# Optimization experiments

Hardware: AMD Instinct MI355X
Metric: run time of the kernel (lower is better)

The kernel has to match this reference:

```python
import jax, jax.numpy as jnp
import numpy as np
from jax import lax

KS, STRIDE, DIL, PAD = 3, 1, 1, 1
B, C_IN, C_OUT, D = 1, 16, 16, 64
K = KS ** 3


def setup_inputs():
    key = jax.random.key(0)
    k1, k2, k3 = jax.random.split(key, 3)
    x = jax.random.normal(k1, (B, C_IN, D, D, D), jnp.float32)
    std = 1.0 / float(np.sqrt(C_IN * K))
    kernel = jax.random.uniform(k2, (K, C_IN, C_OUT), jnp.float32, -std, std)
    # module zero-inits pkernel; use small random values so interp path is exercised
    pkernel = jax.random.normal(k3, (K, C_IN, 3 * K), jnp.float32) * 0.01
    return {"x": x, "kernel": kernel, "pkernel": pkernel}


def _deform_conv3d(x, kernel, pkernel):
    Bn, C, Dd, H, W = x.shape
    Kt = kernel.shape[0]
    # offset-predicting conv: pkernel [K, C_in, 3K] -> conv weight [3K, C_in, kd, kh, kw]
    w_off = jnp.transpose(pkernel.reshape(KS, KS, KS, C, 3 * Kt), (4, 3, 0, 1, 2))
    off = lax.conv_general_dilated(
        x, w_off, (STRIDE,) * 3, [(PAD, PAD)] * 3,
        rhs_dilation=(DIL,) * 3,
        dimension_numbers=("NCDHW", "OIDHW", "NCDHW"))
    Do, Ho, Wo = off.shape[2], off.shape[3], off.shape[4]
    off = off.reshape(Bn, Kt, 3, Do, Ho, Wo)  # 3 offset coords per kernel tap

    # base sampling grid: out_pos*stride - pad + tap*dilation, then add predicted offset
    r = jnp.arange(KS)
    tap = jnp.stack(jnp.meshgrid(r, r, r, indexing="ij"), -1).reshape(Kt, 3) * DIL - PAD
    gz = (jnp.arange(Do) * STRIDE).astype(x.dtype)
    gy = (jnp.arange(Ho) * STRIDE).astype(x.dtype)
    gx = (jnp.arange(Wo) * STRIDE).astype(x.dtype)
    cz = gz[None, None, :, None, None] + tap[None, :, 0, None, None, None] + off[:, :, 0]
    cy = gy[None, None, None, :, None] + tap[None, :, 1, None, None, None] + off[:, :, 1]
    cx = gx[None, None, None, None, :] + tap[None, :, 2, None, None, None] + off[:, :, 2]

    x_flat = x.reshape(Bn, C, Dd * H * W)

    def gather(idx):  # idx [B,K,Do,Ho,Wo] int32 -> [B,C,K,Do,Ho,Wo]
        g = jax.vmap(lambda xf, ix: xf[:, ix.reshape(-1)])(x_flat, idx)
        return g.reshape(Bn, C, Kt, Do, Ho, Wo)

    z0f = jnp.floor(cz); y0f = jnp.floor(cy); x0f = jnp.floor(cx)
    fz, fy, fx = cz - z0f, cy - y0f, cx - x0f
    z0 = z0f.astype(jnp.int32); y0 = y0f.astype(jnp.int32); x0 = x0f.astype(jnp.int32)

    # trilinear interp: accumulate 8 corners (zero outside volume)
    acc = jnp.zeros((Bn, C, Kt, Do, Ho, Wo), x.dtype)
    for dz in (0, 1):
        for dy in (0, 1):
            for dx in (0, 1):
                zi, yi, xi = z0 + dz, y0 + dy, x0 + dx
                valid = ((zi >= 0) & (zi < Dd) & (yi >= 0) & (yi < H)
                         & (xi >= 0) & (xi < W)).astype(x.dtype)
                w = ((fz if dz else 1.0 - fz) * (fy if dy else 1.0 - fy)
                     * (fx if dx else 1.0 - fx)) * valid
                idx = (jnp.clip(zi, 0, Dd - 1) * (H * W)
                       + jnp.clip(yi, 0, H - 1) * W + jnp.clip(xi, 0, W - 1))
                acc = acc + gather(idx) * w[:, None]

    # weighted sum over taps: kernel [K, C_in, C_out]
    return jnp.einsum("bckdhw,kco->bodhw", acc, kernel)


def reference(x, kernel, pkernel):
    return _deform_conv3d(x, kernel, pkernel)
```

## Files before the change

kernel.cpp:

```cpp
#include <hip/hip_runtime.h>

#define D 64
#define DD 4096
#define DDD 262144
#define K 27

typedef _Float16 half8  __attribute__((ext_vector_type(8)));
typedef _Float16 half2v __attribute__((ext_vector_type(2)));
typedef float    f32x4  __attribute__((ext_vector_type(4)));
typedef float    f32x2  __attribute__((ext_vector_type(2)));
typedef float    f32x16 __attribute__((ext_vector_type(16)));

#define HX 12
#define HY 8
#define HZ 6
#define HROW 12
#define HPLN 96
#define HSP  576
#define CPAD 24
#define VSLOT 24

#define WSW_CH (14*6*64)
#define KSW_CH (27*64)
#define KSW_OFF 88064

__device__ inline half2v h2of(half8 v, int d) {
    half2v r; r.x = v[2*d]; r.y = v[2*d+1]; return r;
}

__global__ __launch_bounds__(256) void prep_weights(const float* __restrict__ pk,
                                                    const float* __restrict__ kern,
                                                    _Float16* __restrict__ Wsw,
                                                    _Float16* __restrict__ Ksw) {
    int t = blockIdx.x * 256 + threadIdx.x;
    if (t < WSW_CH) {
        int lane = t & 63;
        int sm = t >> 6;
        int s = sm / 6, mt = sm - 6 * s;
        int m = mt * 16 + (lane & 15);
        int q = lane >> 4;
        half8 w;
#pragma unroll
        for (int j = 0; j < 8; ++j) {
            int k = 32 * s + 8 * q + j;
            int kt = k >> 4, c = k & 15;
            float wv = (kt < K && m < 81) ? pk[kt * 1296 + c * 81 + m] : 0.0f;
            w[j] = (_Float16)wv;
        }
        *(half8*)(Wsw + t * 8) = w;
    } else if (t < WSW_CH + KSW_CH) {
        int u = t - WSW_CH;
        int kt = u >> 6, lane = u & 63;
        int m = lane & 31, kh = lane >> 5;
        half8 w;
#pragma unroll
        for (int j = 0; j < 8; ++j) {
            int c = kh * 8 + j;
            float wv = (m < 16) ? kern[kt * 256 + c * 16 + m] : 0.0f;
            w[j] = (_Float16)wv;
        }
        *(half8*)(Ksw + u * 8) = w;
    }
}

__global__ __launch_bounds__(256, 3) void deform_main(
    const float* __restrict__ x,
    const _Float16* __restrict__ Wsw,
    const _Float16* __restrict__ Ksw,
    float* __restrict__ out)
{
    __shared__ _Float16 s_h[HSP * CPAD];
    __shared__ _Float16 s_off[81 * 64];
    __shared__ _Float16 s_v[4 * 64 * VSLOT];

    const int tid  = threadIdx.x;
    const int lane = tid & 63;
    const int wave = __builtin_amdgcn_readfirstlane(tid >> 6);

    const int bx0 = blockIdx.x * 8;
    const int by0 = blockIdx.y * 4;
    const int bz0 = blockIdx.z * 2;

    for (int i = tid; i < HSP; i += 256) {
        int z = i / HPLN;
        int r = i - z * HPLN;
        int y = r / HROW;
        int xx = r - y * HROW;
        int gz = bz0 - 2 + z, gy = by0 - 2 + y, gx = bx0 - 2 + xx;
        bool in = (unsigned)gz < D && (unsigned)gy < D && (unsigned)gx < D;
        half8 a = {}, b = {};
        if (in) {
            const float* p = x + (gz * DD + gy * D + gx);
#pragma unroll
            for (int c = 0; c < 8; ++c) a[c] = (_Float16)p[c * DDD];
#pragma unroll
            for (int c = 0; c < 8; ++c) b[c] = (_Float16)p[(c + 8) * DDD];
        }
        *(half8*)(s_h + i * CPAD)     = a;
        *(half8*)(s_h + i * CPAD + 8) = b;
    }
    __syncthreads();

    {
        const int n = lane & 15, q = lane >> 4;
        const int vtz = wave >> 1;
        const int vty = 2 * (wave & 1) + (n >> 3);
        const int vtx = n & 7;
        f32x4 acc[6] = {};
        for (int s = 0; s < 14; ++s) {
            int kt = 2 * s + (q >> 1);
            int ktc = (kt < K) ? kt : 0;
            int kd = ktc / 9, kh = (ktc / 3) % 3, kw = ktc % 3;
            int idx = (vtz + kd + 1) * HPLN + (vty + kh + 1) * HROW + (vtx + kw + 1);
            half8 bfrag = *(const half8*)(s_h + idx * CPAD + (q & 1) * 8);
#pragma unroll
            for (int mt = 0; mt < 6; ++mt) {
                half8 afrag = *(const half8*)(Wsw + ((s * 6 + mt) * 64 + lane) * 8);
                acc[mt] = __builtin_amdgcn_mfma_f32_16x16x32_f16(afrag, bfrag, acc[mt], 0, 0, 0);
            }
        }
        const int v = wave * 16 + n;
#pragma unroll
        for (int mt = 0; mt < 6; ++mt)
#pragma unroll
            for (int r = 0; r < 4; ++r) {
                int o = mt * 16 + q * 4 + r;
                if (o < 81) s_off[o * 64 + v] = (_Float16)acc[mt][r];
            }
    }
    __syncthreads();

    const int tx = lane & 7, ty = (lane >> 3) & 3, tz = lane >> 5;
    const int gz = bz0 + tz, gy = by0 + ty, gx = bx0 + tx;
    const int l31 = lane & 31, lh = lane >> 5;
    _Float16* sv = s_v + wave * 64 * VSLOT;

    f32x16 acc2[2] = {};

    const int ntaps = (wave < 3) ? 7 : 6;
    for (int t = 0; t < ntaps; ++t) {
        const int kt = wave * 7 + t;
        const int kd = kt / 9, kh = (kt / 3) % 3, kw = kt % 3;
        float cz = (float)(gz + kd - 1) + (float)s_off[(3 * kt + 0) * 64 + lane];
        float cy = (float)(gy + kh - 1) + (float)s_off[(3 * kt + 1) * 64 + lane];
        float cx = (float)(gx + kw - 1) + (float)s_off[(3 * kt + 2) * 64 + lane];
        float zf = floorf(cz), yf = floorf(cy), xf = floorf(cx);
        float fz = cz - zf, fy = cy - yf, fx = cx - xf;
        int z0 = (int)zf, y0 = (int)yf, x0 = (int)xf;
        int hz0 = z0 - bz0 + 2, hy0 = y0 - by0 + 2, hx0 = x0 - bx0 + 2;

        half2v val2[8] = {};
        if ((unsigned)hz0 < (unsigned)(HZ - 1) && (unsigned)hy0 < (unsigned)(HY - 1)
            && (unsigned)hx0 < (unsigned)(HX - 1)) {
#pragma unroll
            for (int dz = 0; dz < 2; ++dz) {
                float wz = dz ? fz : 1.0f - fz;
#pragma unroll
                for (int dy = 0; dy < 2; ++dy) {
                    float wzy = wz * (dy ? fy : 1.0f - fy);
#pragma unroll
                    for (int dx = 0; dx < 2; ++dx) {
                        float w = wzy * (dx ? fx : 1.0f - fx);
                        int idx = (hz0 + dz) * HPLN + (hy0 + dy) * HROW + (hx0 + dx);
                        half8 c0 = *(const half8*)(s_h + idx * CPAD);
                        half8 c1 = *(const half8*)(s_h + idx * CPAD + 8);
                        _Float16 wh = (_Float16)w;
                        half2v w2; w2.x = wh; w2.y = wh;
#pragma unroll
                        for (int d = 0; d < 4; ++d)
                            val2[d] += w2 * h2of(c0, d);
#pragma unroll
                        for (int d = 0; d < 4; ++d)
                            val2[d + 4] += w2 * h2of(c1, d);
                    }
                }
            }
        } else {
            f32x2 valf[8] = {};
#pragma unroll
            for (int dz = 0; dz < 2; ++dz) {
                int zi = z0 + dz;
                float wz = dz ? fz : 1.0f - fz;
#pragma unroll
                for (int dy = 0; dy < 2; ++dy) {
                    int yi = y0 + dy;
                    float wzy = wz * (dy ? fy : 1.0f - fy);
#pragma unroll
                    for (int dx = 0; dx < 2; ++dx) {
                        int xi = x0 + dx;
                        if ((unsigned)zi < D && (unsigned)yi < D && (unsigned)xi < D) {
                            float w = wzy * (dx ? fx : 1.0f - fx);
                            int base = zi * DD + yi * D + xi;
#pragma unroll
                            for (int c = 0; c < 16; ++c)
                                valf[c >> 1][c & 1] += w * x[c * DDD + base];
                        }
                    }
                }
            }
#pragma unroll
            for (int d = 0; d < 8; ++d) {
                val2[d].x = (_Float16)valf[d].x;
                val2[d].y = (_Float16)valf[d].y;
            }
        }

        half8 v0, v1;
#pragma unroll
        for (int d = 0; d < 4; ++d) { v0[2*d] = val2[d].x;     v0[2*d+1] = val2[d].y; }
#pragma unroll
        for (int d = 0; d < 4; ++d) { v1[2*d] = val2[d+4].x;   v1[2*d+1] = val2[d+4].y; }
        *(half8*)(sv + lane * VSLOT)     = v0;
        *(half8*)(sv + lane * VSLOT + 8) = v1;
        asm volatile("s_waitcnt lgkmcnt(0)" ::: "memory");

        half8 af = *(const half8*)(Ksw + (kt * 64 + lane) * 8);
        half8 b0 = *(const half8*)(sv + l31 * VSLOT + lh * 8);
        acc2[0] = __builtin_amdgcn_mfma_f32_32x32x16_f16(af, b0, acc2[0], 0, 0, 0);
        half8 b1 = *(const half8*)(sv + (32 + l31) * VSLOT + lh * 8);
        acc2[1] = __builtin_amdgcn_mfma_f32_32x32x16_f16(af, b1, acc2[1], 0, 0, 0);
        asm volatile("" ::: "memory");
    }

    __syncthreads();
    float* s_red = (float*)s_h;
#pragma unroll
    for (int g = 0; g < 2; ++g)
#pragma unroll
        for (int r = 0; r < 8; ++r) {
            int o = (r & 3) + 8 * (r >> 2) + 4 * lh;
            s_red[(wave * 64 + g * 32 + l31) * 17 + o] = acc2[g][r];
        }
    __syncthreads();

#pragma unroll
    for (int j = 0; j < 4; ++j) {
        int o = wave * 4 + j;
        float s = s_red[(0 * 64 + lane) * 17 + o]
                + s_red[(1 * 64 + lane) * 17 + o]
                + s_red[(2 * 64 + lane) * 17 + o]
                + s_red[(3 * 64 + lane) * 17 + o];
        out[o * DDD + gz * DD + gy * D + gx] = s;
    }
}

extern "C" void kernel_launch(void* const* d_in, const int* in_sizes, int n_in,
                              void* d_out, int out_size, void* d_ws, size_t ws_size,
                              hipStream_t stream) {
    const float* x    = (const float*)d_in[0];
    const float* kern = (const float*)d_in[1];
    const float* pk   = (const float*)d_in[2];
    float* out = (float*)d_out;

    _Float16* Wsw = (_Float16*)d_ws;
    _Float16* Ksw = (_Float16*)((char*)d_ws + KSW_OFF);

    prep_weights<<<28, 256, 0, stream>>>(pk, kern, Wsw, Ksw);
    deform_main<<<dim3(8, 16, 32), 256, 0, stream>>>(x, Wsw, Ksw, out);
}
```

Baseline: 176.3 us.

## Split channels across lane halves so sampled values feed MFMA directly from registers

Reworks the tap-interpolation phase so each wave takes half the voxels (32) and alternating taps, with the two lane halves each computing 8 of the 16 channels. The interpolated fp16 values then already sit in the B-fragment layout of the 32x32x16 MFMA, which removes the per-wave shared-memory staging buffer, its wait, and the second MFMA per tap. The cross-wave reduction shrinks from four partials to two. Dropping the staging buffer frees LDS, and the launch bound is raised to 4 blocks per SM to gain occupancy, at the cost of a tighter register budget.

Result: faster. 163.8 us (-7.1%).

```diff
diff --git a/kernel.cpp b/kernel.cpp
--- a/kernel.cpp
+++ b/kernel.cpp
@@ -18,7 +18,6 @@
 #define HPLN 96
 #define HSP  576
 #define CPAD 24
-#define VSLOT 24
 
 #define WSW_CH (14*6*64)
 #define KSW_CH (27*64)
@@ -63,7 +62,7 @@
     }
 }
 
-__global__ __launch_bounds__(256, 3) void deform_main(
+__global__ __launch_bounds__(256, 4) void deform_main(
     const float* __restrict__ x,
     const _Float16* __restrict__ Wsw,
     const _Float16* __restrict__ Ksw,
@@ -71,7 +70,6 @@
 {
     __shared__ _Float16 s_h[HSP * CPAD];
     __shared__ _Float16 s_off[81 * 64];
-    __shared__ _Float16 s_v[4 * 64 * VSLOT];
 
     const int tid  = threadIdx.x;
     const int lane = tid & 63;
@@ -130,26 +128,28 @@
     }
     __syncthreads();
 
-    const int tx = lane & 7, ty = (lane >> 3) & 3, tz = lane >> 5;
+    const int l31 = lane & 31, lh = lane >> 5;
+    const int h = wave & 1;
+    const int kpar = wave >> 1;
+    const int v = h * 32 + l31;
+    const int tx = v & 7, ty = (v >> 3) & 3, tz = h;
     const int gz = bz0 + tz, gy = by0 + ty, gx = bx0 + tx;
-    const int l31 = lane & 31, lh = lane >> 5;
-    _Float16* sv = s_v + wave * 64 * VSLOT;
-
-    f32x16 acc2[2] = {};
-
-    const int ntaps = (wave < 3) ? 7 : 6;
-    for (int t = 0; t < ntaps; ++t) {
-        const int kt = wave * 7 + t;
+
+    f32x16 acc2 = {};
+
+    for (int k2 = 0; k2 < 14; ++k2) {
+        const int kt = 2 * k2 + kpar;
+        if (kt >= K) break;
         const int kd = kt / 9, kh = (kt / 3) % 3, kw = kt % 3;
-        float cz = (float)(gz + kd - 1) + (float)s_off[(3 * kt + 0) * 64 + lane];
-        float cy = (float)(gy + kh - 1) + (float)s_off[(3 * kt + 1) * 64 + lane];
-        float cx = (float)(gx + kw - 1) + (float)s_off[(3 * kt + 2) * 64 + lane];
+        float cz = (float)(gz + kd - 1) + (float)s_off[(3 * kt + 0) * 64 + v];
+        float cy = (float)(gy + kh - 1) + (float)s_off[(3 * kt + 1) * 64 + v];
+        float cx = (float)(gx + kw - 1) + (float)s_off[(3 * kt + 2) * 64 + v];
         float zf = floorf(cz), yf = floorf(cy), xf = floorf(cx);
         float fz = cz - zf, fy = cy - yf, fx = cx - xf;
         int z0 = (int)zf, y0 = (int)yf, x0 = (int)xf;
         int hz0 = z0 - bz0 + 2, hy0 = y0 - by0 + 2, hx0 = x0 - bx0 + 2;
 
-        half2v val2[8] = {};
+        half2v val2[4] = {};
         if ((unsigned)hz0 < (unsigned)(HZ - 1) && (unsigned)hy0 < (unsigned)(HY - 1)
             && (unsigned)hx0 < (unsigned)(HX - 1)) {
 #pragma unroll
@@ -162,21 +162,17 @@
                     for (int dx = 0; dx < 2; ++dx) {
                         float w = wzy * (dx ? fx : 1.0f - fx);
                         int idx = (hz0 + dz) * HPLN + (hy0 + dy) * HROW + (hx0 + dx);
-                        half8 c0 = *(const half8*)(s_h + idx * CPAD);
-                        half8 c1 = *(const half8*)(s_h + idx * CPAD + 8);
+                        half8 cc = *(const half8*)(s_h + idx * CPAD + lh * 8);
                         _Float16 wh = (_Float16)w;
                         half2v w2; w2.x = wh; w2.y = wh;
 #pragma unroll
                         for (int d = 0; d < 4; ++d)
-                            val2[d] += w2 * h2of(c0, d);
-#pragma unroll
-                        for (int d = 0; d < 4; ++d)
-                            val2[d + 4] += w2 * h2of(c1, d);
+                            val2[d] += w2 * h2of(cc, d);
                     }
                 }
             }
         } else {
-            f32x2 valf[8] = {};
+            f32x2 valf[4] = {};
 #pragma unroll
             for (int dz = 0; dz < 2; ++dz) {
                 int zi = z0 + dz;
@@ -192,55 +188,43 @@
                             float w = wzy * (dx ? fx : 1.0f - fx);
                             int base = zi * DD + yi * D + xi;
 #pragma unroll
-                            for (int c = 0; c < 16; ++c)
-                                valf[c >> 1][c & 1] += w * x[c * DDD + base];
+                            for (int d = 0; d < 4; ++d) {
+                                valf[d].x += w * x[(lh * 8 + 2 * d)     * DDD + base];
+                                valf[d].y += w * x[(lh * 8 + 2 * d + 1) * DDD + base];
+                            }
                         }
                     }
                 }
             }
 #pragma unroll
-            for (int d = 0; d < 8; ++d) {
+            for (int d = 0; d < 4; ++d) {
                 val2[d].x = (_Float16)valf[d].x;
                 val2[d].y = (_Float16)valf[d].y;
             }
         }
 
-        half8 v0, v1;
-#pragma unroll
-        for (int d = 0; d < 4; ++d) { v0[2*d] = val2[d].x;     v0[2*d+1] = val2[d].y; }
-#pragma unroll
-        for (int d = 0; d < 4; ++d) { v1[2*d] = val2[d+4].x;   v1[2*d+1] = val2[d+4].y; }
-        *(half8*)(sv + lane * VSLOT)     = v0;
-        *(half8*)(sv + lane * VSLOT + 8) = v1;
-        asm volatile("s_waitcnt lgkmcnt(0)" ::: "memory");
-
+        half8 bf;
+#pragma unroll
+        for (int d = 0; d < 4; ++d) { bf[2*d] = val2[d].x; bf[2*d+1] = val2[d].y; }
         half8 af = *(const half8*)(Ksw + (kt * 64 + lane) * 8);
-        half8 b0 = *(const half8*)(sv + l31 * VSLOT + lh * 8);
-        acc2[0] = __builtin_amdgcn_mfma_f32_32x32x16_f16(af, b0, acc2[0], 0, 0, 0);
-        half8 b1 = *(const half8*)(sv + (32 + l31) * VSLOT + lh * 8);
-        acc2[1] = __builtin_amdgcn_mfma_f32_32x32x16_f16(af, b1, acc2[1], 0, 0, 0);
-        asm volatile("" ::: "memory");
+        acc2 = __builtin_amdgcn_mfma_f32_32x32x16_f16(af, bf, acc2, 0, 0, 0);
     }
 
     __syncthreads();
     float* s_red = (float*)s_h;
 #pragma unroll
-    for (int g = 0; g < 2; ++g)
-#pragma unroll
-        for (int r = 0; r < 8; ++r) {
-            int o = (r & 3) + 8 * (r >> 2) + 4 * lh;
-            s_red[(wave * 64 + g * 32 + l31) * 17 + o] = acc2[g][r];
-        }
+    for (int r = 0; r < 8; ++r) {
+        int o = (r & 3) + 8 * (r >> 2) + 4 * lh;
+        s_red[(wave * 32 + l31) * 17 + o] = acc2[r];
+    }
     __syncthreads();
 
 #pragma unroll
     for (int j = 0; j < 4; ++j) {
         int o = wave * 4 + j;
-        float s = s_red[(0 * 64 + lane) * 17 + o]
-                + s_red[(1 * 64 + lane) * 17 + o]
-                + s_red[(2 * 64 + lane) * 17 + o]
-                + s_red[(3 * 64 + lane) * 17 + o];
-        out[o * DDD + gz * DD + gy * D + gx] = s;
+        float s = s_red[lane * 17 + o] + s_red[(64 + lane) * 17 + o];
+        out[o * DDD + (bz0 + (lane >> 5)) * DD + (by0 + ((lane >> 3) & 3)) * D
+            + (bx0 + (lane & 7))] = s;
     }
 }
 
```
